# Optimization experiments

Measured on AMD Instinct MI355X. Metric: run time of the kernel, lower is better.

Reference implementation:

```python
import jax, jax.numpy as jnp
import numpy as np

H = 64      # hidden_size
IN = 4800   # input_size
DEPTH = 14  # complete binary tree depth -> N = 2**DEPTH - 1 nodes


def setup_inputs() -> dict:
    key = jax.random.key(0)
    ks = jax.random.split(key, 10)
    N = 2 ** DEPTH - 1
    s = 0.02
    return {
        "inputs": jax.random.normal(ks[0], (N, IN), jnp.float32),
        # stacked gate weights [i; f; o; u], torch Linear convention y = x @ W.T + b
        "Wx_w": jax.random.normal(ks[1], (4 * H, IN), jnp.float32) * s,
        "Wx_b": jax.random.normal(ks[2], (4 * H,), jnp.float32) * s,
        "U_i": jax.random.normal(ks[3], (H, H), jnp.float32) * s,
        "U_f": jax.random.normal(ks[4], (H, H), jnp.float32) * s,
        "U_o": jax.random.normal(ks[5], (H, H), jnp.float32) * s,
        "U_u": jax.random.normal(ks[6], (H, H), jnp.float32) * s,
        # Conv2d(1, H, (2, H)) kernel squeezed to [out=H, kh=2, kw=H]
        "convW": jax.random.normal(ks[7], (H, 2, H), jnp.float32) * s,
        "conv_b": jax.random.normal(ks[8], (H,), jnp.float32) * s,
        "depth": DEPTH,
    }


def reference(inputs, Wx_w, Wx_b, U_i, U_f, U_o, U_u, convW, conv_b, depth):
    # Precompute all input-side gate projections in one GEMM: [N, 4H]
    Wx = inputs @ Wx_w.T + Wx_b
    Xi, Xf, Xo, Xu = jnp.split(Wx, 4, axis=-1)
    h_below = c_below = None
    # Bottom-up over tree levels (fixed small count; nodes within a level vectorized)
    for d in range(depth - 1, -1, -1):
        n = 2 ** d
        start = 2 ** d - 1  # level-order offset
        xi, xf, xo, xu = (a[start:start + n] for a in (Xi, Xf, Xo, Xu))
        if d == depth - 1:
            # Leaves: single zero child state duplicated twice -> conv of zeros = bias;
            # sum_f term is f * c_child = f * 0 = 0.
            avg = jnp.broadcast_to(conv_b, (n, H))
            sum_f = jnp.zeros((n, H), inputs.dtype)
        else:
            ch_h = h_below.reshape(n, 2, H)  # children hidden states
            ch_c = c_below.reshape(n, 2, H)  # children cell states
            # Conv2d over [1,1,2,H] child tensor -> one spatial position; max over it is identity
            avg = jnp.einsum('okh,nkh->no', convW, ch_h) + conv_b
            # forget gate per child: sigmoid(W_f x + U_f h_k)
            f = jax.nn.sigmoid(xf[:, None, :] + jnp.einsum('nkh,oh->nko', ch_h, U_f))
            sum_f = jnp.sum(f * ch_c, axis=1)
        i = jax.nn.sigmoid(xi + avg @ U_i.T)
        o = jax.nn.sigmoid(xo + avg @ U_o.T)
        u = jnp.tanh(xu + avg @ U_u.T)
        c = sum_f + i * u
        h = o * jnp.tanh(c)
        h_below, c_below = h, c
    # Root (hidden_state, cell_memory), each [1, H] (batch_size = 1)
    return h_below, c_below
```

## Files before the change

### kernel.cpp

```cpp
#include <hip/hip_runtime.h>
#include <math.h>

#define H 64
#define IN_DIM 4800
#define DEPTH 14
#define NNODES ((1 << DEPTH) - 1)

typedef __attribute__((ext_vector_type(8))) short short8;
typedef __attribute__((ext_vector_type(4))) float f32x4;

__global__ void convert_w(const float* __restrict__ W, ushort* __restrict__ Wh,
                          ushort* __restrict__ Wl, int n4)
{
    int i = blockIdx.x * blockDim.x + threadIdx.x;
    if (i >= n4) return;
    float4 v = *(const float4*)&W[i * 4];
    float xs[4] = {v.x, v.y, v.z, v.w};
    ushort hv[4], lv[4];
#pragma unroll
    for (int j = 0; j < 4; ++j) {
        unsigned xb = __float_as_uint(xs[j]);
        hv[j] = (ushort)(xb >> 16);
        float r = xs[j] - __uint_as_float(xb & 0xFFFF0000u);
        lv[j] = (ushort)(__float_as_uint(r) >> 16);
    }
    *(ushort4*)&Wh[i * 4] = make_ushort4(hv[0], hv[1], hv[2], hv[3]);
    *(ushort4*)&Wl[i * 4] = make_ushort4(lv[0], lv[1], lv[2], lv[3]);
}

#define BM 64
#define BN 128
#define BK 32
#define NT (IN_DIM / BK)

__global__ __launch_bounds__(256, 2) void gemm_split(
    const float* __restrict__ A,
    const ushort* __restrict__ Bh, const ushort* __restrict__ Bl,
    const float* __restrict__ bias, float* __restrict__ C)
{
    __shared__ ushort Ah_s[BM][BK];
    __shared__ ushort Al_s[BM][BK];
    __shared__ ushort Bh_s[BN][BK];
    __shared__ ushort Bl_s[BN][BK];

    const int tid  = threadIdx.x;
    const int wave = tid >> 6, lane = tid & 63;
    const int wm = wave >> 1, wn = wave & 1;
    const int m0 = blockIdx.y * BM;
    const int n0 = blockIdx.x * BN;

    const int ar = tid >> 2, ac = (tid & 3) * 8;
    const int aRowC = (m0 + ar < NNODES) ? (m0 + ar) : (NNODES - 1);
    const float* aPtr = A + (size_t)aRowC * IN_DIM + ac;
    const int br = tid >> 2, bc = (tid & 3) * 8;
    const ushort* bhPtr = Bh + (size_t)(n0 + br) * IN_DIM + bc;
    const ushort* blPtr = Bl + (size_t)(n0 + br) * IN_DIM + bc;

    f32x4 acc[2][4] = {};

    float4 a_reg0, a_reg1;
    short8 bh_reg0, bh_reg1, bl_reg0, bl_reg1;

#define LOAD_TILE(t)                                                          \
    {                                                                         \
        const int k0 = (t) * BK;                                              \
        a_reg0 = *(const float4*)(aPtr + k0);                                 \
        a_reg1 = *(const float4*)(aPtr + k0 + 4);                             \
        bh_reg0 = *(const short8*)(bhPtr + k0);                               \
        bh_reg1 = *(const short8*)(bhPtr + (size_t)64 * IN_DIM + k0);         \
        bl_reg0 = *(const short8*)(blPtr + k0);                               \
        bl_reg1 = *(const short8*)(blPtr + (size_t)64 * IN_DIM + k0);         \
    }

#define WRITE_TILE()                                                          \
    {                                                                         \
        float xs[8] = {a_reg0.x, a_reg0.y, a_reg0.z, a_reg0.w,                \
                       a_reg1.x, a_reg1.y, a_reg1.z, a_reg1.w};               \
        short8 hv, lv;                                                        \
        _Pragma("unroll")                                                     \
        for (int j = 0; j < 8; ++j) {                                         \
            unsigned xb = __float_as_uint(xs[j]);                             \
            hv[j] = (short)(xb >> 16);                                        \
            float r = xs[j] - __uint_as_float(xb & 0xFFFF0000u);              \
            lv[j] = (short)(__float_as_uint(r) >> 16);                        \
        }                                                                     \
        *(short8*)&Ah_s[ar][ac] = hv;                                         \
        *(short8*)&Al_s[ar][ac] = lv;                                         \
        *(short8*)&Bh_s[br][bc] = bh_reg0;                                    \
        *(short8*)&Bh_s[64 + br][bc] = bh_reg1;                               \
        *(short8*)&Bl_s[br][bc] = bl_reg0;                                    \
        *(short8*)&Bl_s[64 + br][bc] = bl_reg1;                               \
    }

    LOAD_TILE(0);
    WRITE_TILE();
    __syncthreads();

    const int fr = lane & 15, kg = (lane >> 4) * 8;

    for (int t = 0; t < NT; ++t) {
        if (t + 1 < NT) LOAD_TILE(t + 1);

        short8 ah[2], al[2], bh[4], bl[4];
#pragma unroll
        for (int mf = 0; mf < 2; ++mf) {
            int r = wm * 32 + mf * 16 + fr;
            ah[mf] = *(const short8*)&Ah_s[r][kg];
            al[mf] = *(const short8*)&Al_s[r][kg];
        }
#pragma unroll
        for (int nf = 0; nf < 4; ++nf) {
            int r = wn * 64 + nf * 16 + fr;
            bh[nf] = *(const short8*)&Bh_s[r][kg];
            bl[nf] = *(const short8*)&Bl_s[r][kg];
        }
#pragma unroll
        for (int mf = 0; mf < 2; ++mf)
#pragma unroll
            for (int nf = 0; nf < 4; ++nf) {
                acc[mf][nf] = __builtin_amdgcn_mfma_f32_16x16x32_bf16(ah[mf], bh[nf], acc[mf][nf], 0, 0, 0);
                acc[mf][nf] = __builtin_amdgcn_mfma_f32_16x16x32_bf16(ah[mf], bl[nf], acc[mf][nf], 0, 0, 0);
                acc[mf][nf] = __builtin_amdgcn_mfma_f32_16x16x32_bf16(al[mf], bh[nf], acc[mf][nf], 0, 0, 0);
            }
        __syncthreads();
        if (t + 1 < NT) { WRITE_TILE(); __syncthreads(); }
    }

    const int rquad = (lane >> 4) * 4;
#pragma unroll
    for (int nf = 0; nf < 4; ++nf) {
        int n = n0 + wn * 64 + nf * 16 + fr;
        float bv = bias[n];
#pragma unroll
        for (int mf = 0; mf < 2; ++mf) {
            int mbase = m0 + wm * 32 + mf * 16 + rquad;
#pragma unroll
            for (int j = 0; j < 4; ++j) {
                int m = mbase + j;
                if (m < NNODES)
                    C[(size_t)m * 256 + n] = acc[mf][nf][j] + bv;
            }
        }
    }
#undef LOAD_TILE
#undef WRITE_TILE
}

__device__ __forceinline__ float sigmoidf_(float x) { return 1.0f / (1.0f + expf(-x)); }

__global__ __launch_bounds__(256) void level_kernel(
    const float* __restrict__ Wx,
    const float* __restrict__ convW,
    const float* __restrict__ conv_b,
    const float* __restrict__ Ui, const float* __restrict__ Uf,
    const float* __restrict__ Uo, const float* __restrict__ Uu,
    float* __restrict__ harr, float* __restrict__ carr,
    int base, int n, int isLeaf)
{
    __shared__ float sh[4][192];
    const int wave = threadIdx.x >> 6;
    const int lane = threadIdx.x & 63;
    const int node = blockIdx.x * 4 + wave;
    const bool active = node < n;
    const int idx = base + node;

    float xi = 0.f, xf = 0.f, xo = 0.f, xu = 0.f;
    float avg = 0.f, sumf = 0.f, cl = 0.f, cr = 0.f;

    if (active) {
        xi = Wx[idx * 256 + lane];
        xf = Wx[idx * 256 + 64 + lane];
        xo = Wx[idx * 256 + 128 + lane];
        xu = Wx[idx * 256 + 192 + lane];
        avg = conv_b[lane];
        if (!isLeaf) {
            int li = 2 * idx + 1, ri = 2 * idx + 2;
            float hl = harr[li * 64 + lane];
            float hr = harr[ri * 64 + lane];
            cl = carr[li * 64 + lane];
            cr = carr[ri * 64 + lane];
            sh[wave][lane] = hl;
            sh[wave][64 + lane] = hr;
        }
    }
    __syncthreads();

    if (active && !isLeaf) {
        float fa_l = 0.f, fa_r = 0.f;
#pragma unroll
        for (int t4 = 0; t4 < 16; ++t4) {
            float4 vl = *(const float4*)&sh[wave][t4 * 4];
            float4 vr = *(const float4*)&sh[wave][64 + t4 * 4];
            float4 w0 = *(const float4*)&convW[lane * 128 + t4 * 4];
            float4 w1 = *(const float4*)&convW[lane * 128 + 64 + t4 * 4];
            float4 uf = *(const float4*)&Uf[lane * 64 + t4 * 4];
            avg += w0.x * vl.x + w0.y * vl.y + w0.z * vl.z + w0.w * vl.w;
            avg += w1.x * vr.x + w1.y * vr.y + w1.z * vr.z + w1.w * vr.w;
            fa_l += uf.x * vl.x + uf.y * vl.y + uf.z * vl.z + uf.w * vl.w;
            fa_r += uf.x * vr.x + uf.y * vr.y + uf.z * vr.z + uf.w * vr.w;
        }
        float fl = sigmoidf_(xf + fa_l);
        float fr = sigmoidf_(xf + fa_r);
        sumf = fl * cl + fr * cr;
    }

    if (active) sh[wave][128 + lane] = avg;
    __syncthreads();

    if (active) {
        float ai = 0.f, ao = 0.f, au = 0.f;
#pragma unroll
        for (int t4 = 0; t4 < 16; ++t4) {
            float4 v  = *(const float4*)&sh[wave][128 + t4 * 4];
            float4 wi = *(const float4*)&Ui[lane * 64 + t4 * 4];
            float4 wo = *(const float4*)&Uo[lane * 64 + t4 * 4];
            float4 wu = *(const float4*)&Uu[lane * 64 + t4 * 4];
            ai += wi.x * v.x + wi.y * v.y + wi.z * v.z + wi.w * v.w;
            ao += wo.x * v.x + wo.y * v.y + wo.z * v.z + wo.w * v.w;
            au += wu.x * v.x + wu.y * v.y + wu.z * v.z + wu.w * v.w;
        }
        float iv = sigmoidf_(xi + ai);
        float ov = sigmoidf_(xo + ao);
        float uv = tanhf(xu + au);
        float cv = sumf + iv * uv;
        float hv = ov * tanhf(cv);
        harr[idx * 64 + lane] = hv;
        carr[idx * 64 + lane] = cv;
    }
}

__global__ void out_kernel(const float* __restrict__ h, const float* __restrict__ c,
                           float* __restrict__ out)
{
    int t = threadIdx.x;
    if (t < 64) out[t] = h[t];
    else out[t] = c[t - 64];
}

extern "C" void kernel_launch(void* const* d_in, const int* in_sizes, int n_in,
                              void* d_out, int out_size, void* d_ws, size_t ws_size,
                              hipStream_t stream)
{
    const float* inputs = (const float*)d_in[0];
    const float* Wx_w   = (const float*)d_in[1];
    const float* Wx_b   = (const float*)d_in[2];
    const float* Ui     = (const float*)d_in[3];
    const float* Uf     = (const float*)d_in[4];
    const float* Uo     = (const float*)d_in[5];
    const float* Uu     = (const float*)d_in[6];
    const float* convW  = (const float*)d_in[7];
    const float* conv_b = (const float*)d_in[8];

    float*  Wx = (float*)d_ws;
    float*  h  = (float*)((char*)d_ws + (size_t)(20u << 20));
    float*  c  = (float*)((char*)d_ws + (size_t)(25u << 20));
    ushort* Wh = (ushort*)((char*)d_ws + (size_t)(30u << 20));
    ushort* Wl = (ushort*)((char*)d_ws + (size_t)(33u << 20));

    convert_w<<<1200, 256, 0, stream>>>(Wx_w, Wh, Wl, 307200);

    dim3 ggrid(2, 256);
    gemm_split<<<ggrid, 256, 0, stream>>>(inputs, Wh, Wl, Wx_b, Wx);

    for (int d = DEPTH - 1; d >= 0; --d) {
        int n = 1 << d;
        int base = n - 1;
        int blocks = (n + 3) >> 2;
        level_kernel<<<blocks, 256, 0, stream>>>(Wx, convW, conv_b, Ui, Uf, Uo, Uu,
                                                 h, c, base, n, (d == DEPTH - 1) ? 1 : 0);
    }

    out_kernel<<<1, 128, 0, stream>>>(h, c, (float*)d_out);
}
```

Before: 811.8 us.

## Fuse tree levels into persistent grid-synced kernel and narrow GEMM N tile

Replaces the 14 per-level launches and the output-copy kernel with one persistent kernel of 256 blocks. The blocks step through the tree levels using an atomic grid barrier, and the kernel writes the root state straight to the output. Leaf nodes now use a precomputed U·conv_b term instead of the full matvecs. The input-projection GEMM tile shrinks from 128 to 64 columns with higher occupancy, which gives more blocks but makes each block reread the A rows more times. The grid barrier assumes all 256 blocks are resident at once, and per-wave shared-memory reuse relies on in-wave ordering without explicit barriers.

```diff
diff --git a/kernel.cpp b/kernel.cpp
--- a/kernel.cpp
+++ b/kernel.cpp
@@ -5,6 +5,7 @@
 #define IN_DIM 4800
 #define DEPTH 14
 #define NNODES ((1 << DEPTH) - 1)
+#define NWAVES 1024
 
 typedef __attribute__((ext_vector_type(8))) short short8;
 typedef __attribute__((ext_vector_type(4))) float f32x4;
@@ -29,11 +30,11 @@
 }
 
 #define BM 64
-#define BN 128
+#define BN 64
 #define BK 32
 #define NT (IN_DIM / BK)
 
-__global__ __launch_bounds__(256, 2) void gemm_split(
+__global__ __launch_bounds__(256, 4) void gemm_split(
     const float* __restrict__ A,
     const ushort* __restrict__ Bh, const ushort* __restrict__ Bl,
     const float* __restrict__ bias, float* __restrict__ C)
@@ -56,10 +57,10 @@
     const ushort* bhPtr = Bh + (size_t)(n0 + br) * IN_DIM + bc;
     const ushort* blPtr = Bl + (size_t)(n0 + br) * IN_DIM + bc;
 
-    f32x4 acc[2][4] = {};
+    f32x4 acc[2][2] = {};
 
     float4 a_reg0, a_reg1;
-    short8 bh_reg0, bh_reg1, bl_reg0, bl_reg1;
+    short8 bh_reg0, bl_reg0;
 
 #define LOAD_TILE(t)                                                          \
     {                                                                         \
@@ -67,9 +68,7 @@
         a_reg0 = *(const float4*)(aPtr + k0);                                 \
         a_reg1 = *(const float4*)(aPtr + k0 + 4);                             \
         bh_reg0 = *(const short8*)(bhPtr + k0);                               \
-        bh_reg1 = *(const short8*)(bhPtr + (size_t)64 * IN_DIM + k0);         \
         bl_reg0 = *(const short8*)(blPtr + k0);                               \
-        bl_reg1 = *(const short8*)(blPtr + (size_t)64 * IN_DIM + k0);         \
     }
 
 #define WRITE_TILE()                                                          \
@@ -87,9 +86,7 @@
         *(short8*)&Ah_s[ar][ac] = hv;                                         \
         *(short8*)&Al_s[ar][ac] = lv;                                         \
         *(short8*)&Bh_s[br][bc] = bh_reg0;                                    \
-        *(short8*)&Bh_s[64 + br][bc] = bh_reg1;                               \
         *(short8*)&Bl_s[br][bc] = bl_reg0;                                    \
-        *(short8*)&Bl_s[64 + br][bc] = bl_reg1;                               \
     }
 
     LOAD_TILE(0);
@@ -101,7 +98,7 @@
     for (int t = 0; t < NT; ++t) {
         if (t + 1 < NT) LOAD_TILE(t + 1);
 
-        short8 ah[2], al[2], bh[4], bl[4];
+        short8 ah[2], al[2], bh[2], bl[2];
 #pragma unroll
         for (int mf = 0; mf < 2; ++mf) {
             int r = wm * 32 + mf * 16 + fr;
@@ -109,15 +106,15 @@
             al[mf] = *(const short8*)&Al_s[r][kg];
         }
 #pragma unroll
-        for (int nf = 0; nf < 4; ++nf) {
-            int r = wn * 64 + nf * 16 + fr;
+        for (int nf = 0; nf < 2; ++nf) {
+            int r = wn * 32 + nf * 16 + fr;
             bh[nf] = *(const short8*)&Bh_s[r][kg];
             bl[nf] = *(const short8*)&Bl_s[r][kg];
         }
 #pragma unroll
         for (int mf = 0; mf < 2; ++mf)
 #pragma unroll
-            for (int nf = 0; nf < 4; ++nf) {
+            for (int nf = 0; nf < 2; ++nf) {
                 acc[mf][nf] = __builtin_amdgcn_mfma_f32_16x16x32_bf16(ah[mf], bh[nf], acc[mf][nf], 0, 0, 0);
                 acc[mf][nf] = __builtin_amdgcn_mfma_f32_16x16x32_bf16(ah[mf], bl[nf], acc[mf][nf], 0, 0, 0);
                 acc[mf][nf] = __builtin_amdgcn_mfma_f32_16x16x32_bf16(al[mf], bh[nf], acc[mf][nf], 0, 0, 0);
@@ -128,8 +125,8 @@
 
     const int rquad = (lane >> 4) * 4;
 #pragma unroll
-    for (int nf = 0; nf < 4; ++nf) {
-        int n = n0 + wn * 64 + nf * 16 + fr;
+    for (int nf = 0; nf < 2; ++nf) {
+        int n = n0 + wn * 32 + nf * 16 + fr;
         float bv = bias[n];
 #pragma unroll
         for (int mf = 0; mf < 2; ++mf) {
@@ -146,95 +143,128 @@
 #undef WRITE_TILE
 }
 
+__global__ void init_bar(unsigned* bar) { bar[0] = 0u; bar[1] = 0u; }
+
 __device__ __forceinline__ float sigmoidf_(float x) { return 1.0f / (1.0f + expf(-x)); }
 
-__global__ __launch_bounds__(256) void level_kernel(
+__device__ __forceinline__ void grid_sync(unsigned* count, unsigned* gen)
+{
+    __threadfence();
+    __syncthreads();
+    if (threadIdx.x == 0) {
+        unsigned g = __hip_atomic_load(gen, __ATOMIC_RELAXED, __HIP_MEMORY_SCOPE_AGENT);
+        unsigned old = __hip_atomic_fetch_add(count, 1u, __ATOMIC_ACQ_REL, __HIP_MEMORY_SCOPE_AGENT);
+        if (old == gridDim.x - 1) {
+            __hip_atomic_store(count, 0u, __ATOMIC_RELAXED, __HIP_MEMORY_SCOPE_AGENT);
+            __hip_atomic_fetch_add(gen, 1u, __ATOMIC_RELEASE, __HIP_MEMORY_SCOPE_AGENT);
+        } else {
+            while (__hip_atomic_load(gen, __ATOMIC_ACQUIRE, __HIP_MEMORY_SCOPE_AGENT) == g)
+                __builtin_amdgcn_s_sleep(2);
+        }
+    }
+    __syncthreads();
+    __threadfence();
+}
+
+__global__ __launch_bounds__(256, 1) void tree_kernel(
     const float* __restrict__ Wx,
     const float* __restrict__ convW,
     const float* __restrict__ conv_b,
     const float* __restrict__ Ui, const float* __restrict__ Uf,
     const float* __restrict__ Uo, const float* __restrict__ Uu,
     float* __restrict__ harr, float* __restrict__ carr,
-    int base, int n, int isLeaf)
+    float* __restrict__ out, unsigned* __restrict__ bar)
 {
     __shared__ float sh[4][192];
     const int wave = threadIdx.x >> 6;
     const int lane = threadIdx.x & 63;
-    const int node = blockIdx.x * 4 + wave;
-    const bool active = node < n;
-    const int idx = base + node;
-
-    float xi = 0.f, xf = 0.f, xo = 0.f, xu = 0.f;
-    float avg = 0.f, sumf = 0.f, cl = 0.f, cr = 0.f;
-
-    if (active) {
-        xi = Wx[idx * 256 + lane];
-        xf = Wx[idx * 256 + 64 + lane];
-        xo = Wx[idx * 256 + 128 + lane];
-        xu = Wx[idx * 256 + 192 + lane];
-        avg = conv_b[lane];
-        if (!isLeaf) {
+    const int gw = blockIdx.x * 4 + wave;
+
+    float cli = 0.f, clo = 0.f, clu = 0.f;
+#pragma unroll
+    for (int t4 = 0; t4 < 16; ++t4) {
+        float4 cb = *(const float4*)&conv_b[t4 * 4];
+        float4 wi = *(const float4*)&Ui[lane * 64 + t4 * 4];
+        float4 wo = *(const float4*)&Uo[lane * 64 + t4 * 4];
+        float4 wu = *(const float4*)&Uu[lane * 64 + t4 * 4];
+        cli += wi.x * cb.x + wi.y * cb.y + wi.z * cb.z + wi.w * cb.w;
+        clo += wo.x * cb.x + wo.y * cb.y + wo.z * cb.z + wo.w * cb.w;
+        clu += wu.x * cb.x + wu.y * cb.y + wu.z * cb.z + wu.w * cb.w;
+    }
+
+    {
+        const int n = 1 << (DEPTH - 1), base = n - 1;
+        for (int node = gw; node < n; node += NWAVES) {
+            int idx = base + node;
+            float xi = Wx[idx * 256 + lane];
+            float xo = Wx[idx * 256 + 128 + lane];
+            float xu = Wx[idx * 256 + 192 + lane];
+            float iv = sigmoidf_(xi + cli);
+            float ov = sigmoidf_(xo + clo);
+            float uv = tanhf(xu + clu);
+            float cv = iv * uv;
+            float hv = ov * tanhf(cv);
+            harr[idx * 64 + lane] = hv;
+            carr[idx * 64 + lane] = cv;
+        }
+    }
+
+    for (int d = DEPTH - 2; d >= 0; --d) {
+        grid_sync(&bar[0], &bar[1]);
+        const int n = 1 << d, base = n - 1;
+        for (int node = gw; node < n; node += NWAVES) {
+            int idx = base + node;
+            float xi = Wx[idx * 256 + lane];
+            float xf = Wx[idx * 256 + 64 + lane];
+            float xo = Wx[idx * 256 + 128 + lane];
+            float xu = Wx[idx * 256 + 192 + lane];
             int li = 2 * idx + 1, ri = 2 * idx + 2;
-            float hl = harr[li * 64 + lane];
-            float hr = harr[ri * 64 + lane];
-            cl = carr[li * 64 + lane];
-            cr = carr[ri * 64 + lane];
-            sh[wave][lane] = hl;
-            sh[wave][64 + lane] = hr;
-        }
-    }
-    __syncthreads();
-
-    if (active && !isLeaf) {
-        float fa_l = 0.f, fa_r = 0.f;
-#pragma unroll
-        for (int t4 = 0; t4 < 16; ++t4) {
-            float4 vl = *(const float4*)&sh[wave][t4 * 4];
-            float4 vr = *(const float4*)&sh[wave][64 + t4 * 4];
-            float4 w0 = *(const float4*)&convW[lane * 128 + t4 * 4];
-            float4 w1 = *(const float4*)&convW[lane * 128 + 64 + t4 * 4];
-            float4 uf = *(const float4*)&Uf[lane * 64 + t4 * 4];
-            avg += w0.x * vl.x + w0.y * vl.y + w0.z * vl.z + w0.w * vl.w;
-            avg += w1.x * vr.x + w1.y * vr.y + w1.z * vr.z + w1.w * vr.w;
-            fa_l += uf.x * vl.x + uf.y * vl.y + uf.z * vl.z + uf.w * vl.w;
-            fa_r += uf.x * vr.x + uf.y * vr.y + uf.z * vr.z + uf.w * vr.w;
-        }
-        float fl = sigmoidf_(xf + fa_l);
-        float fr = sigmoidf_(xf + fa_r);
-        sumf = fl * cl + fr * cr;
-    }
-
-    if (active) sh[wave][128 + lane] = avg;
-    __syncthreads();
-
-    if (active) {
-        float ai = 0.f, ao = 0.f, au = 0.f;
-#pragma unroll
-        for (int t4 = 0; t4 < 16; ++t4) {
-            float4 v  = *(const float4*)&sh[wave][128 + t4 * 4];
-            float4 wi = *(const float4*)&Ui[lane * 64 + t4 * 4];
-            float4 wo = *(const float4*)&Uo[lane * 64 + t4 * 4];
-            float4 wu = *(const float4*)&Uu[lane * 64 + t4 * 4];
-            ai += wi.x * v.x + wi.y * v.y + wi.z * v.z + wi.w * v.w;
-            ao += wo.x * v.x + wo.y * v.y + wo.z * v.z + wo.w * v.w;
-            au += wu.x * v.x + wu.y * v.y + wu.z * v.z + wu.w * v.w;
-        }
-        float iv = sigmoidf_(xi + ai);
-        float ov = sigmoidf_(xo + ao);
-        float uv = tanhf(xu + au);
-        float cv = sumf + iv * uv;
-        float hv = ov * tanhf(cv);
-        harr[idx * 64 + lane] = hv;
-        carr[idx * 64 + lane] = cv;
-    }
-}
-
-__global__ void out_kernel(const float* __restrict__ h, const float* __restrict__ c,
-                           float* __restrict__ out)
-{
-    int t = threadIdx.x;
-    if (t < 64) out[t] = h[t];
-    else out[t] = c[t - 64];
+            float cl = carr[li * 64 + lane];
+            float cr = carr[ri * 64 + lane];
+            sh[wave][lane]      = harr[li * 64 + lane];
+            sh[wave][64 + lane] = harr[ri * 64 + lane];
+            float avg = conv_b[lane], fa_l = 0.f, fa_r = 0.f;
+#pragma unroll
+            for (int t4 = 0; t4 < 16; ++t4) {
+                float4 vl = *(const float4*)&sh[wave][t4 * 4];
+                float4 vr = *(const float4*)&sh[wave][64 + t4 * 4];
+                float4 w0 = *(const float4*)&convW[lane * 128 + t4 * 4];
+                float4 w1 = *(const float4*)&convW[lane * 128 + 64 + t4 * 4];
+                float4 uf = *(const float4*)&Uf[lane * 64 + t4 * 4];
+                avg  += w0.x * vl.x + w0.y * vl.y + w0.z * vl.z + w0.w * vl.w;
+                avg  += w1.x * vr.x + w1.y * vr.y + w1.z * vr.z + w1.w * vr.w;
+                fa_l += uf.x * vl.x + uf.y * vl.y + uf.z * vl.z + uf.w * vl.w;
+                fa_r += uf.x * vr.x + uf.y * vr.y + uf.z * vr.z + uf.w * vr.w;
+            }
+            float fl = sigmoidf_(xf + fa_l);
+            float fr = sigmoidf_(xf + fa_r);
+            float sumf = fl * cl + fr * cr;
+
+            sh[wave][128 + lane] = avg;
+            float ai = 0.f, ao = 0.f, au = 0.f;
+#pragma unroll
+            for (int t4 = 0; t4 < 16; ++t4) {
+                float4 v  = *(const float4*)&sh[wave][128 + t4 * 4];
+                float4 wi = *(const float4*)&Ui[lane * 64 + t4 * 4];
+                float4 wo = *(const float4*)&Uo[lane * 64 + t4 * 4];
+                float4 wu = *(const float4*)&Uu[lane * 64 + t4 * 4];
+                ai += wi.x * v.x + wi.y * v.y + wi.z * v.z + wi.w * v.w;
+                ao += wo.x * v.x + wo.y * v.y + wo.z * v.z + wo.w * v.w;
+                au += wu.x * v.x + wu.y * v.y + wu.z * v.z + wu.w * v.w;
+            }
+            float iv = sigmoidf_(xi + ai);
+            float ov = sigmoidf_(xo + ao);
+            float uv = tanhf(xu + au);
+            float cv = sumf + iv * uv;
+            float hv = ov * tanhf(cv);
+            harr[idx * 64 + lane] = hv;
+            carr[idx * 64 + lane] = cv;
+            if (idx == 0) {
+                out[lane] = hv;
+                out[64 + lane] = cv;
+            }
+        }
+    }
 }
 
 extern "C" void kernel_launch(void* const* d_in, const int* in_sizes, int n_in,
@@ -251,24 +281,21 @@
     const float* convW  = (const float*)d_in[7];
     const float* conv_b = (const float*)d_in[8];
 
-    float*  Wx = (float*)d_ws;
-    float*  h  = (float*)((char*)d_ws + (size_t)(20u << 20));
-    float*  c  = (float*)((char*)d_ws + (size_t)(25u << 20));
-    ushort* Wh = (ushort*)((char*)d_ws + (size_t)(30u << 20));
-    ushort* Wl = (ushort*)((char*)d_ws + (size_t)(33u << 20));
-
+    float*    Wx  = (float*)d_ws;
+    float*    h   = (float*)((char*)d_ws + (size_t)(16u << 20));
+    float*    c   = (float*)((char*)d_ws + (size_t)(20u << 20));
+    ushort*   Wh  = (ushort*)((char*)d_ws + (size_t)(24u << 20));
+    ushort*   Wl  = (ushort*)((char*)d_ws + (size_t)(27u << 20));
+    unsigned* bar = (unsigned*)((char*)d_ws + (size_t)(30u << 20));
+
+    init_bar<<<1, 1, 0, stream>>>(bar);
     convert_w<<<1200, 256, 0, stream>>>(Wx_w, Wh, Wl, 307200);
 
-    dim3 ggrid(2, 256);
-    gemm_split<<<ggrid, 256, 0, stream>>>(inputs, Wh, Wl, Wx_b, Wx);
-
-    for (int d = DEPTH - 1; d >= 0; --d) {
-        int n = 1 << d;
-        int base = n - 1;
-        int blocks = (n + 3) >> 2;
-        level_kernel<<<blocks, 256, 0, stream>>>(Wx, convW, conv_b, Ui, Uf, Uo, Uu,
-                                                 h, c, base, n, (d == DEPTH - 1) ? 1 : 0);
-    }
-
-    out_kernel<<<1, 128, 0, stream>>>(h, c, (float*)d_out);
-}
+    dim3 ggrid(1, 256);
+    ggrid.x = 256 / BN * 4 / 4;
+    ggrid.x = 4;
+    gemm_split<<<dim3(4, 256), 256, 0, stream>>>(inputs, Wh, Wl, Wx_b, Wx);
+
+    tree_kernel<<<256, 256, 0, stream>>>(Wx, convW, conv_b, Ui, Uf, Uo, Uu,
+                                         h, c, (float*)d_out, bar);
+}
```

Result: slower. 2.193 ms (+170.2%).
